# Kernel tuning notes

Measured on AMD Instinct MI355X. Metric: run time of the kernel, lower is better.

The kernel has to match this reference:

```python
import jax, jax.numpy as jnp
import numpy as np

NUM_HEADS = 8


def setup_inputs() -> dict:
    key = jax.random.key(0)
    ks = jax.random.split(key, 16)
    B, Ct, Co, H, W = 1, 256, 128, 64, 64
    s = lambda k, *shape: jax.random.normal(k, shape, dtype=jnp.float32) * 0.02
    return {
        "thermal_features": jax.random.normal(ks[0], (B, Ct, H, W), dtype=jnp.float32),
        "optical_features": jax.random.normal(ks[1], (B, Co, H, W), dtype=jnp.float32),
        "emissivity_map": jax.random.uniform(ks[2], (B, 1, H, W), dtype=jnp.float32),
        "Wq": s(ks[3], Ct, Ct), "bq": jnp.zeros((Ct,), jnp.float32),
        "Wk": s(ks[4], Ct, Co), "bk": jnp.zeros((Ct,), jnp.float32),
        "Wv": s(ks[5], Ct, Co), "bv": jnp.zeros((Ct,), jnp.float32),
        "conv1_w": s(ks[6], 32, 1, 3, 3), "conv1_b": jnp.zeros((32,), jnp.float32),
        "conv2_w": s(ks[7], NUM_HEADS, 32, 1, 1), "conv2_b": jnp.zeros((NUM_HEADS,), jnp.float32),
        "Wp": s(ks[8], Ct, Ct), "bp": jnp.zeros((Ct,), jnp.float32),
    }


def reference(thermal_features, optical_features, emissivity_map,
              Wq, bq, Wk, bk, Wv, bv, conv1_w, conv1_b, conv2_w, conv2_b, Wp, bp):
    B, Ct, H, W = thermal_features.shape
    Co = optical_features.shape[1]
    N = H * W
    h = NUM_HEADS
    d = Ct // h
    scale = d ** (-0.5)

    # flatten spatial -> tokens: [B, N, C]
    t_flat = thermal_features.reshape(B, Ct, N).transpose(0, 2, 1)
    o_flat = optical_features.reshape(B, Co, N).transpose(0, 2, 1)

    # projections, split heads: [B, h, N, d]
    q = (t_flat @ Wq.T + bq).reshape(B, N, h, d).transpose(0, 2, 1, 3)
    k = (o_flat @ Wk.T + bk).reshape(B, N, h, d).transpose(0, 2, 1, 3)
    v = (o_flat @ Wv.T + bv).reshape(B, N, h, d).transpose(0, 2, 1, 3)

    # full attention scores: [B, h, N, N]
    attn = jnp.einsum('bhqd,bhkd->bhqk', q, k) * scale

    # emissivity gate: Conv(1->32, 3x3, pad 1) -> ReLU -> Conv(32->h, 1x1) -> Sigmoid
    g = jax.lax.conv_general_dilated(emissivity_map, conv1_w, (1, 1), 'SAME',
                                     dimension_numbers=('NCHW', 'OIHW', 'NCHW'))
    g = jax.nn.relu(g + conv1_b[None, :, None, None])
    g = jax.lax.conv_general_dilated(g, conv2_w, (1, 1), 'SAME',
                                     dimension_numbers=('NCHW', 'OIHW', 'NCHW'))
    g = jax.nn.sigmoid(g + conv2_b[None, :, None, None])  # [B, h, H, W]
    g = g.reshape(B, h, N)[..., None]  # [B, h, N, 1] gates query rows

    attn = jax.nn.softmax(attn * g, axis=-1)  # dropout is identity in eval

    out = jnp.einsum('bhqk,bhkd->bhqd', attn, v)  # [B, h, N, d]
    out = out.transpose(0, 2, 1, 3).reshape(B, N, Ct)
    out = out @ Wp.T + bp
    return out.transpose(0, 2, 1).reshape(B, Ct, H, W)
```

## Files before the change

### kernel.cpp

```cpp
#include <hip/hip_runtime.h>
#include <hip/hip_bf16.h>

#define N_TOK 4096
#define CT 256

typedef __attribute__((ext_vector_type(8))) short bf16x8;
typedef __attribute__((ext_vector_type(16))) float f32x16;

__device__ __forceinline__ unsigned pkbf(float a, float b) {
  float2 t; t.x = a; t.y = b;
  __hip_bfloat162 h = __float22bfloat162_rn(t);
  return *reinterpret_cast<unsigned*>(&h);
}

#if __has_builtin(__builtin_amdgcn_exp2f)
__device__ __forceinline__ float fexp2(float x) { return __builtin_amdgcn_exp2f(x); }
#else
__device__ __forceinline__ float fexp2(float x) { return exp2f(x); }
#endif

__global__ __launch_bounds__(256) void prep_kernel(
    const float* __restrict__ thermal, const float* __restrict__ optical,
    const float* __restrict__ Wq, const float* __restrict__ Wk,
    const float* __restrict__ Wv, const float* __restrict__ Wp,
    const float* __restrict__ em, const float* __restrict__ w1,
    const float* __restrict__ b1, const float* __restrict__ w2,
    const float* __restrict__ b2,
    unsigned short* __restrict__ Xbt, unsigned short* __restrict__ Xbo,
    unsigned short* __restrict__ Wall, float* __restrict__ g)
{
  __shared__ unsigned short tile[64][264];
  const int bx = blockIdx.x, tid = threadIdx.x;
  if (bx < 128) {
    const bool th = (bx < 64);
    const float* X = th ? thermal : optical;
    unsigned short* Xb = th ? Xbt : Xbo;
    const int CIN = th ? 256 : 128;
    const int n0 = (th ? bx : bx - 64) * 64;
    const int nl = tid & 63;
    const int cw = (tid >> 6) * 4;
    for (int c0 = 0; c0 < CIN; c0 += 16) {
      int c = c0 + cw;
      float x0 = X[(size_t)(c + 0) * N_TOK + n0 + nl];
      float x1 = X[(size_t)(c + 1) * N_TOK + n0 + nl];
      float x2 = X[(size_t)(c + 2) * N_TOK + n0 + nl];
      float x3 = X[(size_t)(c + 3) * N_TOK + n0 + nl];
      uint2 w; w.x = pkbf(x0, x1); w.y = pkbf(x2, x3);
      *(uint2*)&tile[nl][c] = w;
    }
    __syncthreads();
    const int n = tid >> 2, q = tid & 3;
    const int cb = q * (CIN / 4);
    for (int j = 0; j < CIN / 4; j += 4)
      *(uint2*)(Xb + (size_t)(n0 + n) * CIN + cb + j) = *(const uint2*)&tile[n][cb + j];
  } else if (bx < 224) {
    int i = (bx - 128) * 2048 + tid * 8;
    const float* src; int off;
    if (i < 65536)       { src = Wq; off = 0; }
    else if (i < 98304)  { src = Wk; off = 65536; }
    else if (i < 131072) { src = Wv; off = 98304; }
    else                 { src = Wp; off = 131072; }
    float4 f0 = *(const float4*)(src + (i - off));
    float4 f1 = *(const float4*)(src + (i - off) + 4);
    uint4 o;
    o.x = pkbf(f0.x, f0.y); o.y = pkbf(f0.z, f0.w);
    o.z = pkbf(f1.x, f1.y); o.w = pkbf(f1.z, f1.w);
    *(uint4*)(Wall + i) = o;
  } else {
    int n = (bx - 224) * 256 + tid;
    int y = n >> 6, x = n & 63;
    float e[9];
#pragma unroll
    for (int dy = 0; dy < 3; dy++)
#pragma unroll
      for (int dx = 0; dx < 3; dx++) {
        int yy = y + dy - 1, xx = x + dx - 1;
        e[dy * 3 + dx] = (yy >= 0 && yy < 64 && xx >= 0 && xx < 64)
                             ? em[yy * 64 + xx] : 0.f;
      }
    float c1[32];
#pragma unroll
    for (int oc = 0; oc < 32; oc++) {
      float a = b1[oc];
#pragma unroll
      for (int t = 0; t < 9; t++) a = fmaf(e[t], w1[oc * 9 + t], a);
      c1[oc] = fmaxf(a, 0.f);
    }
#pragma unroll
    for (int hh = 0; hh < 8; hh++) {
      float a = b2[hh];
#pragma unroll
      for (int oc = 0; oc < 32; oc++) a = fmaf(c1[oc], w2[hh * 32 + oc], a);
      g[hh * N_TOK + n] = 1.f / (1.f + __expf(-a));
    }
  }
}

template <int CIN>
__device__ __forceinline__ void gemm_tile(
    const unsigned short* __restrict__ xp, const unsigned short* __restrict__ wp,
    f32x16& accE, f32x16& accO)
{
#pragma unroll
  for (int c = 0; c < CIN; c += 32) {
    bf16x8 a0 = *(const bf16x8*)(xp + c);
    bf16x8 b0 = *(const bf16x8*)(wp + c);
    bf16x8 a1 = *(const bf16x8*)(xp + c + 16);
    bf16x8 b1 = *(const bf16x8*)(wp + c + 16);
    accE = __builtin_amdgcn_mfma_f32_32x32x16_bf16(a0, b0, accE, 0, 0, 0);
    accO = __builtin_amdgcn_mfma_f32_32x32x16_bf16(a1, b1, accO, 0, 0, 0);
  }
}

__global__ __launch_bounds__(256) void qkv_kernel(
    const unsigned short* __restrict__ Xbt, const unsigned short* __restrict__ Xbo,
    const unsigned short* __restrict__ Wall,
    const float* __restrict__ bq, const float* __restrict__ bk,
    const float* __restrict__ bv, const float* __restrict__ g,
    unsigned short* __restrict__ Qh, unsigned short* __restrict__ Kh,
    unsigned short* __restrict__ Vf)
{
  __shared__ float ldsT[4][32][33];
  const int tid = threadIdx.x;
  const int wave = tid >> 6, lane = tid & 63;
  const int l31 = lane & 31, hi = lane >> 5;
  const int y = blockIdx.y;
  const int head = y & 7;
  const int n0 = blockIdx.x * 128 + wave * 32;

  f32x16 accE, accO;
#pragma unroll
  for (int i = 0; i < 16; i++) { accE[i] = 0.f; accO[i] = 0.f; }
  float bo;
  if (y < 8) {
    gemm_tile<256>(Xbt + (size_t)(n0 + l31) * 256 + hi * 8,
                   Wall + (size_t)(head * 32 + l31) * 256 + hi * 8, accE, accO);
    bo = bq[head * 32 + l31];
  } else if (y < 16) {
    gemm_tile<128>(Xbo + (size_t)(n0 + l31) * 128 + hi * 8,
                   Wall + 65536 + (size_t)(head * 32 + l31) * 128 + hi * 8, accE, accO);
    bo = bk[head * 32 + l31];
  } else {
    gemm_tile<128>(Xbo + (size_t)(n0 + l31) * 128 + hi * 8,
                   Wall + 98304 + (size_t)(head * 32 + l31) * 128 + hi * 8, accE, accO);
    bo = bv[head * 32 + l31];
  }
  float val[16];
#pragma unroll
  for (int r = 0; r < 16; r++) val[r] = accE[r] + accO[r] + bo;

  if (y < 8) {
    const float QSC = 0.17677669529663689f * 1.4426950408889634f;
#pragma unroll
    for (int r = 0; r < 16; r++) {
      int t = n0 + (r & 3) + 8 * (r >> 2) + 4 * hi;
      val[r] *= QSC * g[head * N_TOK + t];
    }
  }
#pragma unroll
  for (int r = 0; r < 16; r++)
    ldsT[wave][(r & 3) + 8 * (r >> 2) + 4 * hi][l31] = val[r];

  if (y < 16) {
    unsigned pk[8];
#pragma unroll
    for (int i = 0; i < 8; i++)
      pk[i] = pkbf(ldsT[wave][l31][16 * hi + 2 * i],
                   ldsT[wave][l31][16 * hi + 2 * i + 1]);
    unsigned short* dst = (y < 8 ? Qh : Kh) +
        ((size_t)head * N_TOK + n0 + l31) * 32 + 16 * hi;
    *(uint4*)dst = make_uint4(pk[0], pk[1], pk[2], pk[3]);
    *(uint4*)(dst + 8) = make_uint4(pk[4], pk[5], pk[6], pk[7]);
  } else {
    unsigned pk[8];
#pragma unroll
    for (int i = 0; i < 8; i++)
      pk[i] = pkbf(ldsT[wave][16 * hi + 2 * i][l31],
                   ldsT[wave][16 * hi + 2 * i + 1][l31]);
    unsigned short* dst = Vf +
        (((size_t)head * 256 + (n0 >> 4) + hi) * 32 + l31) * 16;
    *(uint4*)dst = make_uint4(pk[0], pk[1], pk[2], pk[3]);
    *(uint4*)(dst + 8) = make_uint4(pk[4], pk[5], pk[6], pk[7]);
  }
}

__global__ __launch_bounds__(256, 4) void attn_kernel(
    const unsigned short* __restrict__ Qh, const unsigned short* __restrict__ Kh,
    const unsigned short* __restrict__ Vf, unsigned short* __restrict__ Ab)
{
  __shared__ float combA[4][32][33];
  __shared__ float combL[4][32];
  const int tid = threadIdx.x;
  const int wave = tid >> 6, lane = tid & 63;
  const int l31 = lane & 31, hi = lane >> 5;
  const int hh = blockIdx.x & 7;
  const int qb = blockIdx.x >> 3;
  const int qrow0 = qb * 32;
  const int kbase0 = wave * 1024;

  const unsigned short* qrow = Qh + ((size_t)hh * N_TOK + qrow0 + l31) * 32;
  const bf16x8 qf0 = *(const bf16x8*)(qrow + hi * 8);
  const bf16x8 qf1 = *(const bf16x8*)(qrow + 16 + hi * 8);

  const unsigned short* kb_base = Kh + (size_t)hh * (N_TOK * 32);
  const unsigned short* vf_base = Vf + (size_t)hh * (256 * 32 * 16);

  f32x16 acc, zero16;
#pragma unroll
  for (int i = 0; i < 16; i++) { acc[i] = 0.f; zero16[i] = 0.f; }
  float lsum = 0.f;

#define LK(kb, s) (*(const bf16x8*)(kb_base + (size_t)((kb) + l31) * 32 + (s) * 16 + hi * 8))
#define LV(kt2)   (*(const bf16x8*)(vf_base + (size_t)((kt2) * 32 + l31) * 16 + hi * 8))

  bf16x8 kf0 = LK(kbase0, 0), kf1 = LK(kbase0, 1);
  bf16x8 vb0 = LV(kbase0 >> 4), vb1 = LV((kbase0 >> 4) + 1);

#pragma unroll 2
  for (int kt = 0; kt < 1024; kt += 32) {
    const int nxt = (kt + 32 < 1024) ? (kbase0 + kt + 32) : kbase0;
    bf16x8 nk0 = LK(nxt, 0), nk1 = LK(nxt, 1);
    bf16x8 nv0 = LV(nxt >> 4), nv1 = LV((nxt >> 4) + 1);

    __builtin_amdgcn_s_setprio(1);
    f32x16 s = __builtin_amdgcn_mfma_f32_32x32x16_bf16(kf0, qf0, zero16, 0, 0, 0);
    s = __builtin_amdgcn_mfma_f32_32x32x16_bf16(kf1, qf1, s, 0, 0, 0);
    __builtin_amdgcn_s_setprio(0);

    float p[16];
#pragma unroll
    for (int r = 0; r < 16; r++) p[r] = fexp2(s[r]);

    lsum += (((p[0] + p[1]) + (p[2] + p[3])) + ((p[4] + p[5]) + (p[6] + p[7]))) +
            (((p[8] + p[9]) + (p[10] + p[11])) + ((p[12] + p[13]) + (p[14] + p[15])));

    unsigned a0 = pkbf(p[0], p[1]),   a1 = pkbf(p[2], p[3]);
    unsigned b0 = pkbf(p[4], p[5]),   b1 = pkbf(p[6], p[7]);
    unsigned c0 = pkbf(p[8], p[9]),   c1 = pkbf(p[10], p[11]);
    unsigned d0 = pkbf(p[12], p[13]), d1 = pkbf(p[14], p[15]);
    asm("v_permlane32_swap_b32 %0, %1" : "+v"(a0), "+v"(b0));
    asm("v_permlane32_swap_b32 %0, %1" : "+v"(a1), "+v"(b1));
    asm("v_permlane32_swap_b32 %0, %1" : "+v"(c0), "+v"(d0));
    asm("v_permlane32_swap_b32 %0, %1" : "+v"(c1), "+v"(d1));
    union { unsigned w[4]; bf16x8 v; } u0, u1;
    u0.w[0] = a0; u0.w[1] = a1; u0.w[2] = b0; u0.w[3] = b1;
    u1.w[0] = c0; u1.w[1] = c1; u1.w[2] = d0; u1.w[3] = d1;

    __builtin_amdgcn_s_setprio(1);
    acc = __builtin_amdgcn_mfma_f32_32x32x16_bf16(u0.v, vb0, acc, 0, 0, 0);
    acc = __builtin_amdgcn_mfma_f32_32x32x16_bf16(u1.v, vb1, acc, 0, 0, 0);
    __builtin_amdgcn_s_setprio(0);

    kf0 = nk0; kf1 = nk1; vb0 = nv0; vb1 = nv1;
  }
#undef LK
#undef LV

  float lt = lsum + __shfl_xor(lsum, 32);
  if (hi == 0) combL[wave][l31] = lt;

#pragma unroll
  for (int r = 0; r < 16; r++)
    combA[wave][(r & 3) + 8 * (r >> 2) + 4 * hi][l31] = acc[r];
  __syncthreads();

  const int t = tid >> 3;
  const int c4 = (tid & 7) * 4;
  float l = combL[0][t] + combL[1][t] + combL[2][t] + combL[3][t];
  float inv = 1.f / l;
  float o[4];
#pragma unroll
  for (int j = 0; j < 4; j++)
    o[j] = combA[0][t][c4 + j] + combA[1][t][c4 + j] +
           combA[2][t][c4 + j] + combA[3][t][c4 + j];
  uint2 pk;
  pk.x = pkbf(o[0] * inv, o[1] * inv);
  pk.y = pkbf(o[2] * inv, o[3] * inv);
  *(uint2*)(Ab + (size_t)(qrow0 + t) * CT + hh * 32 + c4) = pk;
}

__global__ __launch_bounds__(256, 4) void pout_kernel(
    const unsigned short* __restrict__ Ab, const unsigned short* __restrict__ Wall,
    const float* __restrict__ bp, float* __restrict__ out)
{
  __shared__ float comb[4][32][33];
  const int tid = threadIdx.x;
  const int wave = tid >> 6, lane = tid & 63;
  const int l31 = lane & 31, hi = lane >> 5;
  const int n0 = blockIdx.x * 32;
  const int o0 = blockIdx.y * 32;
  const int cbase = wave * 64;

  const unsigned short* xp = Ab + (size_t)(n0 + l31) * 256 + cbase + hi * 8;
  const unsigned short* wp = Wall + 131072 + (size_t)(o0 + l31) * 256 + cbase + hi * 8;

  f32x16 accE, accO;
#pragma unroll
  for (int i = 0; i < 16; i++) { accE[i] = 0.f; accO[i] = 0.f; }
#pragma unroll
  for (int c = 0; c < 64; c += 32) {
    bf16x8 a0 = *(const bf16x8*)(xp + c);
    bf16x8 b0 = *(const bf16x8*)(wp + c);
    bf16x8 a1 = *(const bf16x8*)(xp + c + 16);
    bf16x8 b1 = *(const bf16x8*)(wp + c + 16);
    accE = __builtin_amdgcn_mfma_f32_32x32x16_bf16(a0, b0, accE, 0, 0, 0);
    accO = __builtin_amdgcn_mfma_f32_32x32x16_bf16(a1, b1, accO, 0, 0, 0);
  }
#pragma unroll
  for (int r = 0; r < 16; r++)
    comb[wave][(r & 3) + 8 * (r >> 2) + 4 * hi][l31] = accE[r] + accO[r];
  __syncthreads();

  const int oc = tid >> 3;
  const int t4 = (tid & 7) * 4;
  const float bo = bp[o0 + oc];
  float4 w;
  w.x = comb[0][t4 + 0][oc] + comb[1][t4 + 0][oc] + comb[2][t4 + 0][oc] + comb[3][t4 + 0][oc] + bo;
  w.y = comb[0][t4 + 1][oc] + comb[1][t4 + 1][oc] + comb[2][t4 + 1][oc] + comb[3][t4 + 1][oc] + bo;
  w.z = comb[0][t4 + 2][oc] + comb[1][t4 + 2][oc] + comb[2][t4 + 2][oc] + comb[3][t4 + 2][oc] + bo;
  w.w = comb[0][t4 + 3][oc] + comb[1][t4 + 3][oc] + comb[2][t4 + 3][oc] + comb[3][t4 + 3][oc] + bo;
  *(float4*)(out + (size_t)(o0 + oc) * N_TOK + n0 + t4) = w;
}

extern "C" void kernel_launch(void* const* d_in, const int* in_sizes, int n_in,
                              void* d_out, int out_size, void* d_ws, size_t ws_size,
                              hipStream_t stream)
{
  const float* thermal = (const float*)d_in[0];
  const float* optical = (const float*)d_in[1];
  const float* em      = (const float*)d_in[2];
  const float* Wq = (const float*)d_in[3];
  const float* bq = (const float*)d_in[4];
  const float* Wk = (const float*)d_in[5];
  const float* bk = (const float*)d_in[6];
  const float* Wv = (const float*)d_in[7];
  const float* bv = (const float*)d_in[8];
  const float* w1 = (const float*)d_in[9];
  const float* b1 = (const float*)d_in[10];
  const float* w2 = (const float*)d_in[11];
  const float* b2 = (const float*)d_in[12];
  const float* Wp = (const float*)d_in[13];
  const float* bp = (const float*)d_in[14];

  char* ws = (char*)d_ws;
  const size_t MB = 1u << 20;
  unsigned short* Xbt = (unsigned short*)(ws);
  unsigned short* Xbo = (unsigned short*)(ws + 2 * MB);
  unsigned short* Wall = (unsigned short*)(ws + 3 * MB);
  float* gbuf = (float*)(ws + 3 * MB + 512 * 1024);
  unsigned short* Qh = (unsigned short*)(ws + 4 * MB);
  unsigned short* Kh = (unsigned short*)(ws + 6 * MB);
  unsigned short* Vf = (unsigned short*)(ws + 8 * MB);
  unsigned short* Ab = (unsigned short*)(ws + 10 * MB);

  prep_kernel<<<240, 256, 0, stream>>>(thermal, optical, Wq, Wk, Wv, Wp,
                                       em, w1, b1, w2, b2, Xbt, Xbo, Wall, gbuf);
  qkv_kernel<<<dim3(32, 24), 256, 0, stream>>>(Xbt, Xbo, Wall, bq, bk, bv, gbuf,
                                               Qh, Kh, Vf);
  attn_kernel<<<1024, 256, 0, stream>>>(Qh, Kh, Vf, Ab);
  pout_kernel<<<dim3(128, 8), 256, 0, stream>>>(Ab, Wall, bp, (float*)d_out);
}
```

Baseline: 59.80 us.

## Process two 32-row query tiles per attention block to reuse K/V loads

```diff
diff --git a/kernel.cpp b/kernel.cpp
--- a/kernel.cpp
+++ b/kernel.cpp
@@ -184,7 +184,7 @@
   }
 }
 
-__global__ __launch_bounds__(256, 4) void attn_kernel(
+__global__ __launch_bounds__(256, 2) void attn_kernel(
     const unsigned short* __restrict__ Qh, const unsigned short* __restrict__ Kh,
     const unsigned short* __restrict__ Vf, unsigned short* __restrict__ Ab)
 {
@@ -195,20 +195,23 @@
   const int l31 = lane & 31, hi = lane >> 5;
   const int hh = blockIdx.x & 7;
   const int qb = blockIdx.x >> 3;
-  const int qrow0 = qb * 32;
+  const int qrow0 = qb * 64;
   const int kbase0 = wave * 1024;
 
-  const unsigned short* qrow = Qh + ((size_t)hh * N_TOK + qrow0 + l31) * 32;
-  const bf16x8 qf0 = *(const bf16x8*)(qrow + hi * 8);
-  const bf16x8 qf1 = *(const bf16x8*)(qrow + 16 + hi * 8);
+  const unsigned short* qrowA = Qh + ((size_t)hh * N_TOK + qrow0 + l31) * 32;
+  const bf16x8 qfA0 = *(const bf16x8*)(qrowA + hi * 8);
+  const bf16x8 qfA1 = *(const bf16x8*)(qrowA + 16 + hi * 8);
+  const unsigned short* qrowB = qrowA + 32 * 32;
+  const bf16x8 qfB0 = *(const bf16x8*)(qrowB + hi * 8);
+  const bf16x8 qfB1 = *(const bf16x8*)(qrowB + 16 + hi * 8);
 
   const unsigned short* kb_base = Kh + (size_t)hh * (N_TOK * 32);
   const unsigned short* vf_base = Vf + (size_t)hh * (256 * 32 * 16);
 
-  f32x16 acc, zero16;
-#pragma unroll
-  for (int i = 0; i < 16; i++) { acc[i] = 0.f; zero16[i] = 0.f; }
-  float lsum = 0.f;
+  f32x16 accA, accB, zero16;
+#pragma unroll
+  for (int i = 0; i < 16; i++) { accA[i] = 0.f; accB[i] = 0.f; zero16[i] = 0.f; }
+  float lsumA = 0.f, lsumB = 0.f;
 
 #define LK(kb, s) (*(const bf16x8*)(kb_base + (size_t)((kb) + l31) * 32 + (s) * 16 + hi * 8))
 #define LV(kt2)   (*(const bf16x8*)(vf_base + (size_t)((kt2) * 32 + l31) * 16 + hi * 8))
@@ -223,32 +226,50 @@
     bf16x8 nv0 = LV(nxt >> 4), nv1 = LV((nxt >> 4) + 1);
 
     __builtin_amdgcn_s_setprio(1);
-    f32x16 s = __builtin_amdgcn_mfma_f32_32x32x16_bf16(kf0, qf0, zero16, 0, 0, 0);
-    s = __builtin_amdgcn_mfma_f32_32x32x16_bf16(kf1, qf1, s, 0, 0, 0);
+    f32x16 sA = __builtin_amdgcn_mfma_f32_32x32x16_bf16(kf0, qfA0, zero16, 0, 0, 0);
+    sA = __builtin_amdgcn_mfma_f32_32x32x16_bf16(kf1, qfA1, sA, 0, 0, 0);
+    f32x16 sB = __builtin_amdgcn_mfma_f32_32x32x16_bf16(kf0, qfB0, zero16, 0, 0, 0);
+    sB = __builtin_amdgcn_mfma_f32_32x32x16_bf16(kf1, qfB1, sB, 0, 0, 0);
     __builtin_amdgcn_s_setprio(0);
 
-    float p[16];
-#pragma unroll
-    for (int r = 0; r < 16; r++) p[r] = fexp2(s[r]);
-
-    lsum += (((p[0] + p[1]) + (p[2] + p[3])) + ((p[4] + p[5]) + (p[6] + p[7]))) +
-            (((p[8] + p[9]) + (p[10] + p[11])) + ((p[12] + p[13]) + (p[14] + p[15])));
-
-    unsigned a0 = pkbf(p[0], p[1]),   a1 = pkbf(p[2], p[3]);
-    unsigned b0 = pkbf(p[4], p[5]),   b1 = pkbf(p[6], p[7]);
-    unsigned c0 = pkbf(p[8], p[9]),   c1 = pkbf(p[10], p[11]);
-    unsigned d0 = pkbf(p[12], p[13]), d1 = pkbf(p[14], p[15]);
-    asm("v_permlane32_swap_b32 %0, %1" : "+v"(a0), "+v"(b0));
-    asm("v_permlane32_swap_b32 %0, %1" : "+v"(a1), "+v"(b1));
-    asm("v_permlane32_swap_b32 %0, %1" : "+v"(c0), "+v"(d0));
-    asm("v_permlane32_swap_b32 %0, %1" : "+v"(c1), "+v"(d1));
-    union { unsigned w[4]; bf16x8 v; } u0, u1;
-    u0.w[0] = a0; u0.w[1] = a1; u0.w[2] = b0; u0.w[3] = b1;
-    u1.w[0] = c0; u1.w[1] = c1; u1.w[2] = d0; u1.w[3] = d1;
+    float pA[16], pB[16];
+#pragma unroll
+    for (int r = 0; r < 16; r++) pA[r] = fexp2(sA[r]);
+#pragma unroll
+    for (int r = 0; r < 16; r++) pB[r] = fexp2(sB[r]);
+
+    lsumA += (((pA[0] + pA[1]) + (pA[2] + pA[3])) + ((pA[4] + pA[5]) + (pA[6] + pA[7]))) +
+             (((pA[8] + pA[9]) + (pA[10] + pA[11])) + ((pA[12] + pA[13]) + (pA[14] + pA[15])));
+    lsumB += (((pB[0] + pB[1]) + (pB[2] + pB[3])) + ((pB[4] + pB[5]) + (pB[6] + pB[7]))) +
+             (((pB[8] + pB[9]) + (pB[10] + pB[11])) + ((pB[12] + pB[13]) + (pB[14] + pB[15])));
+
+    unsigned aA0 = pkbf(pA[0], pA[1]),   aA1 = pkbf(pA[2], pA[3]);
+    unsigned bA0 = pkbf(pA[4], pA[5]),   bA1 = pkbf(pA[6], pA[7]);
+    unsigned cA0 = pkbf(pA[8], pA[9]),   cA1 = pkbf(pA[10], pA[11]);
+    unsigned dA0 = pkbf(pA[12], pA[13]), dA1 = pkbf(pA[14], pA[15]);
+    asm("v_permlane32_swap_b32 %0, %1" : "+v"(aA0), "+v"(bA0));
+    asm("v_permlane32_swap_b32 %0, %1" : "+v"(aA1), "+v"(bA1));
+    asm("v_permlane32_swap_b32 %0, %1" : "+v"(cA0), "+v"(dA0));
+    asm("v_permlane32_swap_b32 %0, %1" : "+v"(cA1), "+v"(dA1));
+    unsigned aB0 = pkbf(pB[0], pB[1]),   aB1 = pkbf(pB[2], pB[3]);
+    unsigned bB0 = pkbf(pB[4], pB[5]),   bB1 = pkbf(pB[6], pB[7]);
+    unsigned cB0 = pkbf(pB[8], pB[9]),   cB1 = pkbf(pB[10], pB[11]);
+    unsigned dB0 = pkbf(pB[12], pB[13]), dB1 = pkbf(pB[14], pB[15]);
+    asm("v_permlane32_swap_b32 %0, %1" : "+v"(aB0), "+v"(bB0));
+    asm("v_permlane32_swap_b32 %0, %1" : "+v"(aB1), "+v"(bB1));
+    asm("v_permlane32_swap_b32 %0, %1" : "+v"(cB0), "+v"(dB0));
+    asm("v_permlane32_swap_b32 %0, %1" : "+v"(cB1), "+v"(dB1));
+    union { unsigned w[4]; bf16x8 v; } uA0, uA1, uB0, uB1;
+    uA0.w[0] = aA0; uA0.w[1] = aA1; uA0.w[2] = bA0; uA0.w[3] = bA1;
+    uA1.w[0] = cA0; uA1.w[1] = cA1; uA1.w[2] = dA0; uA1.w[3] = dA1;
+    uB0.w[0] = aB0; uB0.w[1] = aB1; uB0.w[2] = bB0; uB0.w[3] = bB1;
+    uB1.w[0] = cB0; uB1.w[1] = cB1; uB1.w[2] = dB0; uB1.w[3] = dB1;
 
     __builtin_amdgcn_s_setprio(1);
-    acc = __builtin_amdgcn_mfma_f32_32x32x16_bf16(u0.v, vb0, acc, 0, 0, 0);
-    acc = __builtin_amdgcn_mfma_f32_32x32x16_bf16(u1.v, vb1, acc, 0, 0, 0);
+    accA = __builtin_amdgcn_mfma_f32_32x32x16_bf16(uA0.v, vb0, accA, 0, 0, 0);
+    accA = __builtin_amdgcn_mfma_f32_32x32x16_bf16(uA1.v, vb1, accA, 0, 0, 0);
+    accB = __builtin_amdgcn_mfma_f32_32x32x16_bf16(uB0.v, vb0, accB, 0, 0, 0);
+    accB = __builtin_amdgcn_mfma_f32_32x32x16_bf16(uB1.v, vb1, accB, 0, 0, 0);
     __builtin_amdgcn_s_setprio(0);
 
     kf0 = nk0; kf1 = nk1; vb0 = nv0; vb1 = nv1;
@@ -256,27 +277,49 @@
 #undef LK
 #undef LV
 
-  float lt = lsum + __shfl_xor(lsum, 32);
-  if (hi == 0) combL[wave][l31] = lt;
-
-#pragma unroll
-  for (int r = 0; r < 16; r++)
-    combA[wave][(r & 3) + 8 * (r >> 2) + 4 * hi][l31] = acc[r];
-  __syncthreads();
-
   const int t = tid >> 3;
   const int c4 = (tid & 7) * 4;
-  float l = combL[0][t] + combL[1][t] + combL[2][t] + combL[3][t];
-  float inv = 1.f / l;
-  float o[4];
-#pragma unroll
-  for (int j = 0; j < 4; j++)
-    o[j] = combA[0][t][c4 + j] + combA[1][t][c4 + j] +
-           combA[2][t][c4 + j] + combA[3][t][c4 + j];
-  uint2 pk;
-  pk.x = pkbf(o[0] * inv, o[1] * inv);
-  pk.y = pkbf(o[2] * inv, o[3] * inv);
-  *(uint2*)(Ab + (size_t)(qrow0 + t) * CT + hh * 32 + c4) = pk;
+
+  float ltA = lsumA + __shfl_xor(lsumA, 32);
+  if (hi == 0) combL[wave][l31] = ltA;
+#pragma unroll
+  for (int r = 0; r < 16; r++)
+    combA[wave][(r & 3) + 8 * (r >> 2) + 4 * hi][l31] = accA[r];
+  __syncthreads();
+  {
+    float l = combL[0][t] + combL[1][t] + combL[2][t] + combL[3][t];
+    float inv = 1.f / l;
+    float o[4];
+#pragma unroll
+    for (int j = 0; j < 4; j++)
+      o[j] = combA[0][t][c4 + j] + combA[1][t][c4 + j] +
+             combA[2][t][c4 + j] + combA[3][t][c4 + j];
+    uint2 pk;
+    pk.x = pkbf(o[0] * inv, o[1] * inv);
+    pk.y = pkbf(o[2] * inv, o[3] * inv);
+    *(uint2*)(Ab + (size_t)(qrow0 + t) * CT + hh * 32 + c4) = pk;
+  }
+  __syncthreads();
+
+  float ltB = lsumB + __shfl_xor(lsumB, 32);
+  if (hi == 0) combL[wave][l31] = ltB;
+#pragma unroll
+  for (int r = 0; r < 16; r++)
+    combA[wave][(r & 3) + 8 * (r >> 2) + 4 * hi][l31] = accB[r];
+  __syncthreads();
+  {
+    float l = combL[0][t] + combL[1][t] + combL[2][t] + combL[3][t];
+    float inv = 1.f / l;
+    float o[4];
+#pragma unroll
+    for (int j = 0; j < 4; j++)
+      o[j] = combA[0][t][c4 + j] + combA[1][t][c4 + j] +
+             combA[2][t][c4 + j] + combA[3][t][c4 + j];
+    uint2 pk;
+    pk.x = pkbf(o[0] * inv, o[1] * inv);
+    pk.y = pkbf(o[2] * inv, o[3] * inv);
+    *(uint2*)(Ab + (size_t)(qrow0 + 32 + t) * CT + hh * 32 + c4) = pk;
+  }
 }
 
 __global__ __launch_bounds__(256, 4) void pout_kernel(
@@ -357,6 +400,6 @@
                                        em, w1, b1, w2, b2, Xbt, Xbo, Wall, gbuf);
   qkv_kernel<<<dim3(32, 24), 256, 0, stream>>>(Xbt, Xbo, Wall, bq, bk, bv, gbuf,
                                                Qh, Kh, Vf);
-  attn_kernel<<<1024, 256, 0, stream>>>(Qh, Kh, Vf, Ab);
+  attn_kernel<<<512, 256, 0, stream>>>(Qh, Kh, Vf, Ab);
   pout_kernel<<<dim3(128, 8), 256, 0, stream>>>(Ab, Wall, bp, (float*)d_out);
 }
```

Result: faster. 58.26 us, median of 2 (-2.6%).
